# Performance work log

Measured on AMD Instinct MI355X. Metric: run time of the kernel, lower is better.

## Reference

```python
import jax, jax.numpy as jnp
import numpy as np

HID, HEADS = 2048, 16
HD = HID // HEADS  # head_dim = 128
EPS = 1e-6


def rope_tables(head_dim, max_pos, base=10000.0):
    inv = 1.0 / (base ** (jnp.arange(0, head_dim, 2, dtype=jnp.float32) / head_dim))
    t = jnp.arange(max_pos, dtype=jnp.float32)
    freqs = jnp.outer(t, inv)                      # [max_pos, d/2]
    emb = jnp.concatenate([freqs, freqs], axis=-1)  # [max_pos, d]
    return jnp.cos(emb), jnp.sin(emb)


def rotate_half(x):
    x1, x2 = jnp.split(x, 2, axis=-1)
    return jnp.concatenate([-x2, x1], axis=-1)


def lf_gate(x, c1w, c1b, c2w, c2b, rms_w):
    # x: [b, s, h]; prompt phase -> lf1/lf2 caches are zeros -> zero-pad 1 step on time axis
    xt = jnp.transpose(x, (0, 2, 1))[..., None]                 # [b, h, s, 1]
    xt = jnp.pad(xt, ((0, 0), (0, 0), (1, 0), (0, 0)))           # [b, h, s+1, 1]
    dn = ('NCHW', 'OIHW', 'NCHW')
    o1 = jax.lax.conv_general_dilated(xt, c1w, (1, 1), 'VALID', dimension_numbers=dn)
    o1 = o1 + c1b[None, :, None, None]                           # [b, h/2, s, 1]
    o1 = jnp.pad(o1, ((0, 0), (0, 0), (1, 0), (0, 0)))           # [b, h/2, s+1, 1]
    o2 = jax.lax.conv_general_dilated(o1, c2w, (1, 1), 'VALID', dimension_numbers=dn)
    o2 = o2 + c2b[None, :, None, None]                           # [b, h, s, 1]
    y = jnp.transpose(o2[..., 0], (0, 2, 1)) + x                 # residual, [b, s, h]
    var = jnp.mean(y * y, axis=-1, keepdims=True)
    return y * jax.lax.rsqrt(var + EPS) * rms_w


def setup_inputs() -> dict:
    key = jax.random.key(0)
    ks = jax.random.split(key, 10)
    b, s = 2, 2048
    inp = {
        'hidden_states': jax.random.normal(ks[0], (b, s, HID), jnp.float32),
        'positions': jnp.arange(s, dtype=jnp.int32),
        'wq': jax.random.normal(ks[1], (HID, HID), jnp.float32) * 0.02,
        'wk': jax.random.normal(ks[2], (HID, HID), jnp.float32) * 0.02,
        'wv': jax.random.normal(ks[3], (HID, HID), jnp.float32) * 0.02,
        'wo': jax.random.normal(ks[4], (HID, HID), jnp.float32) * 0.02,
        'conv1_w': jax.random.normal(ks[5], (HID // 2, HID, 2, 1), jnp.float32) * 0.02,
        'conv1_b': jnp.zeros((HID // 2,), jnp.float32),
        'conv2_w': jax.random.normal(ks[6], (HID, HID // 2, 2, 1), jnp.float32) * 0.02,
        'conv2_b': jnp.zeros((HID,), jnp.float32),
        'rms_w': jnp.ones((HID,), jnp.float32),
    }
    return inp


def reference(hidden_states, positions, wq, wk, wv, wo, conv1_w, conv1_b, conv2_w, conv2_b, rms_w):
    b, s, _ = hidden_states.shape
    # value projection from raw hidden states (pre-gate)
    v = (hidden_states @ wv).reshape(b, s, HEADS, HD)            # [b, s, H, d]
    # localized-filtering gate (prompt phase: zero caches)
    h = lf_gate(hidden_states, conv1_w, conv1_b, conv2_w, conv2_b, rms_w)
    q = h @ wq                                                   # [b, s, H*d]
    k = h @ wk
    # faithful Yuan quirk: concat q,k then reshape to [b,s,H,2d] and chunk
    qk = jnp.concatenate([q, k], axis=-1).reshape(b, s, HEADS, 2 * HD)
    q, k = jnp.split(qk, 2, axis=-1)                             # each [b, s, H, d]
    # rotary
    cos, sin = rope_tables(HD, 8192)
    c = cos[positions][None, :, None, :]                         # [1, s, 1, d]
    sn = sin[positions][None, :, None, :]
    q = q * c + rotate_half(q) * sn
    k = k * c + rotate_half(k) * sn
    # causal attention (paged attention reduces to this for the prompt)
    scale = HD ** -0.5
    scores = jnp.einsum('bqhd,bkhd->bhqk', q, k) * scale         # [b, H, s, s]
    mask = jnp.tril(jnp.ones((s, s), dtype=bool))
    scores = jnp.where(mask[None, None], scores, jnp.finfo(scores.dtype).min)
    probs = jax.nn.softmax(scores, axis=-1)
    out = jnp.einsum('bhqk,bkhd->bqhd', probs, v).reshape(b, s, HEADS * HD)
    return out @ wo
```

## Files before the change

### kernel.cpp

```cpp
#include <hip/hip_runtime.h>

#define HID 2048
#define HEADS 16
#define HD 128
#define BATCH 2
#define S 2048
#define ROWS (BATCH*S)

typedef short short8 __attribute__((ext_vector_type(8)));
typedef unsigned short ushort4v __attribute__((ext_vector_type(4)));
typedef unsigned short ushort2v __attribute__((ext_vector_type(2)));
typedef float f32x4 __attribute__((ext_vector_type(4)));
typedef __bf16 bf16x8 __attribute__((ext_vector_type(8)));
typedef __bf16 bf16x4 __attribute__((ext_vector_type(4)));

static __device__ __forceinline__ float b2f(unsigned short u) {
  union { float f; unsigned int i; } v; v.i = ((unsigned int)u) << 16; return v.f;
}
static __device__ __forceinline__ unsigned short f2b(float f) {
  union { float f; unsigned int i; } v; v.f = f;
  unsigned int u = v.i;
  unsigned int r = ((u >> 16) & 1u) + 0x7fffu;
  return (unsigned short)((u + r) >> 16);
}

static __device__ __forceinline__ void gload_lds16(const unsigned short* g, unsigned short* l) {
  __builtin_amdgcn_global_load_lds(
      (const __attribute__((address_space(1))) unsigned int*)(const void*)g,
      (__attribute__((address_space(3))) unsigned int*)(void*)l,
      16, 0, 0);
}

__global__ void fill_debug(unsigned short* __restrict__ out, long n) {
  long i = (long)blockIdx.x * blockDim.x + threadIdx.x;
  if (i < n) out[i] = 0x447A;
}

__global__ void prep_combined(const float* __restrict__ c1w, const float* __restrict__ c2w,
                              const float* __restrict__ x, const int* __restrict__ positions,
                              const float* __restrict__ c1b, const float* __restrict__ c2b,
                              const float* __restrict__ rmsw,
                              const float* __restrict__ wq, const float* __restrict__ wk,
                              const float* __restrict__ wv, const float* __restrict__ wo,
                              unsigned short* __restrict__ w1t0, unsigned short* __restrict__ w1t1,
                              unsigned short* __restrict__ w2t0, unsigned short* __restrict__ w2t1,
                              unsigned short* __restrict__ xb,
                              float* __restrict__ ctab, float* __restrict__ stab,
                              unsigned short* __restrict__ c1bb, unsigned short* __restrict__ c2bb,
                              unsigned short* __restrict__ rmswb, unsigned short* __restrict__ zpg,
                              unsigned short* __restrict__ wqkt, unsigned short* __restrict__ wvt,
                              unsigned short* __restrict__ wot) {
  int job = blockIdx.y;
  if (job == 0 || job == 1) {
    const float* w = (job == 0) ? c1w : c2w;
    unsigned short* o0 = (job == 0) ? w1t0 : w2t0;
    unsigned short* o1 = (job == 0) ? w1t1 : w2t1;
    long i = (long)blockIdx.x * 256 + threadIdx.x;
    f32x4 v = *(const f32x4*)(w + i*4);
    ushort2v a = { f2b(v[0]), f2b(v[2]) };
    ushort2v b = { f2b(v[1]), f2b(v[3]) };
    *(ushort2v*)(o0 + i*2) = a;
    *(ushort2v*)(o1 + i*2) = b;
  } else if (job == 2) {
    long i = (long)blockIdx.x * 256 + threadIdx.x;
    #pragma unroll
    for (int rep = 0; rep < 2; ++rep) {
      long idx = i + (long)rep * 1048576L;
      f32x4 v = *(const f32x4*)(x + idx*4);
      ushort4v o = { f2b(v[0]), f2b(v[1]), f2b(v[2]), f2b(v[3]) };
      *(ushort4v*)(xb + idx*4) = o;
    }
  } else if (job == 3) {
    int bx = blockIdx.x;
    if (bx < 512) {
      int t = bx * 4 + (threadIdx.x >> 6);
      int i = threadIdx.x & 63;
      float pos = (float)positions[t];
      float inv = powf(10000.0f, -(float)i / 64.0f);
      float ang = pos * inv;
      float sv, cv;
      sincosf(ang, &sv, &cv);
      ctab[t*64 + i] = cv;
      stab[t*64 + i] = sv;
    } else if (bx < 544) {
      int i = (bx - 512) * 256 + threadIdx.x;
      if (i < 1024) c1bb[i] = f2b(c1b[i]);
      if (i < 2048) { c2bb[i] = f2b(c2b[i]); rmswb[i] = f2b(rmsw[i]); }
      zpg[i] = 0;
    }
  } else {
    __shared__ unsigned short tl[64][73];
    int bx = blockIdx.x;
    int mat = bx >> 10;
    int tx = (bx >> 5) & 31, ty = bx & 31;
    const float* in; unsigned short* out; int perm;
    switch (mat) {
      case 0:  in = wq; out = wqkt;                       perm = 1; break;
      case 1:  in = wk; out = wqkt + (size_t)HID*HID;     perm = 1; break;
      case 2:  in = wv; out = wvt;                        perm = 0; break;
      default: in = wo; out = wot;                        perm = 0; break;
    }
    int n0 = tx * 64, k0 = ty * 64;
    int tid = threadIdx.x;
    int r = tid >> 3, c8 = (tid & 7) * 8;
    #pragma unroll
    for (int j = 0; j < 2; ++j) {
      int rr = r + j*32;
      const float* p = in + (size_t)(k0 + rr)*HID + n0 + c8;
      f32x4 v0 = *(const f32x4*)p;
      f32x4 v1 = *(const f32x4*)(p + 4);
      #pragma unroll
      for (int e = 0; e < 4; ++e) { tl[rr][c8 + e] = f2b(v0[e]); tl[rr][c8 + 4 + e] = f2b(v1[e]); }
    }
    __syncthreads();
    #pragma unroll
    for (int j = 0; j < 2; ++j) {
      int rr = r + j*32;
      int orow = n0 + rr;
      if (perm) {
        int s5 = (orow >> 5) & 3;
        s5 = (s5 == 1) ? 2 : (s5 == 2) ? 1 : s5;
        orow = (orow & ~127) | (s5 << 5) | (orow & 31);
      }
      short8 v;
      #pragma unroll
      for (int e = 0; e < 8; ++e) v[e] = (short)tl[c8 + e][rr];
      *(short8*)(out + (size_t)orow*HID + k0 + c8) = v;
    }
  }
}


static __device__ __forceinline__ int swz_scol(int lane) {
  return (((lane & 7) * 16) ^ (((lane >> 3) & 7) << 4)) >> 1;
}

static __device__ __forceinline__ void rd_af(const unsigned short* Ah, bf16x8 (&afr)[4][2],
                                             int wm, int lr, int col0, int axor) {
  #pragma unroll
  for (int mi = 0; mi < 4; ++mi) {
    const unsigned short* rp = Ah + (wm*64 + mi*16 + lr) * 64;
    #pragma unroll
    for (int kk = 0; kk < 2; ++kk)
      afr[mi][kk] = *(const bf16x8*)(rp + (((kk*64 + col0) ^ axor) >> 1));
  }
}
static __device__ __forceinline__ void rd_bf(const unsigned short* Bh, bf16x8 (&bfr)[2][2],
                                             int wn, int lr, int col0, int axor) {
  #pragma unroll
  for (int ni = 0; ni < 2; ++ni) {
    const unsigned short* rp = Bh + (wn*32 + ni*16 + lr) * 64;
    #pragma unroll
    for (int kk = 0; kk < 2; ++kk)
      bfr[ni][kk] = *(const bf16x8*)(rp + (((kk*64 + col0) ^ axor) >> 1));
  }
}
static __device__ __forceinline__ void mfma16(const bf16x8 (&afr)[4][2], const bf16x8 (&bfr)[2][2],
                                              f32x4 (&ac)[4][2]) {
  #pragma unroll
  for (int kk = 0; kk < 2; ++kk)
    #pragma unroll
    for (int mi = 0; mi < 4; ++mi)
      #pragma unroll
      for (int ni = 0; ni < 2; ++ni)
        ac[mi][ni] = __builtin_amdgcn_mfma_f32_16x16x32_bf16(afr[mi][kk], bfr[ni][kk], ac[mi][ni], 0, 0, 0);
}


struct SPtrs { const unsigned short* p[6]; };

static __device__ __forceinline__ void build_ptrs(SPtrs& sp,
    const unsigned short* Ap, const unsigned short* Bp, int Ksz, int sh,
    int m0, int n0, const unsigned short* zpg, int tid) {
  int lane = tid & 63;
  int scol = swz_scol(lane);
  #pragma unroll
  for (int j = 0; j < 2; ++j) {
    int row = ((tid >> 6) * 2 + j) * 8 + (lane >> 3);
    int gr = m0 + row;
    sp.p[j]     = (sh && ((gr & (S - 1)) == 0)) ? (zpg + scol)
                                                : (Ap + (size_t)(gr - sh)*Ksz + scol);
    sp.p[2 + j] = Bp + (size_t)(n0 + row)*Ksz + scol;
    sp.p[4 + j] = Bp + (size_t)(n0 + 128 + row)*Ksz + scol;
  }
}

static __device__ __forceinline__ void stage6(unsigned short* buf, SPtrs& sp, int tid) {
  int c0 = (tid >> 6) * 1024;
  gload_lds16(sp.p[0], buf + c0);
  gload_lds16(sp.p[1], buf + c0 + 512);
  gload_lds16(sp.p[2], buf + 8192  + c0);
  gload_lds16(sp.p[3], buf + 8192  + c0 + 512);
  gload_lds16(sp.p[4], buf + 16384 + c0);
  gload_lds16(sp.p[5], buf + 16384 + c0 + 512);
  #pragma unroll
  for (int i = 0; i < 6; ++i) sp.p[i] += 64;
}

static __device__ __forceinline__ void gemm8_core(
    unsigned short* lds,
    const unsigned short* __restrict__ A1, const unsigned short* __restrict__ A2,
    const unsigned short* __restrict__ B1, const unsigned short* __restrict__ B2,
    int K1, int K2,
    const unsigned short* __restrict__ bias, const unsigned short* __restrict__ resid,
    void* __restrict__ Cout, int outmode, int N, int m0, int n0,
    int a1shift, const unsigned short* __restrict__ zrow) {
  int tid = threadIdx.x;
  int lane = tid & 63, w = tid >> 6;
  int wm = w >> 2, wn = w & 3;
  int lr = lane & 15, g = lane >> 4;
  int col0 = g * 16;
  int axor = (lr & 7) << 4;
  int nk1 = K1 >> 6;
  int nk = (K1 + K2) >> 6;
  f32x4 acc[2][4][2] = {};
  bf16x8 afr[4][2], bfr0[2][2], bfr1[2][2];

  unsigned short* buf0 = lds;
  unsigned short* buf1 = lds + 24576;
  unsigned short* buf2 = lds + 49152;

  SPtrs sp;
  build_ptrs(sp, A1, B1, K1, a1shift, m0, n0, zrow, tid);

  stage6(buf0, sp, tid);
  stage6(buf1, sp, tid);

  unsigned short* cur = buf0;
  unsigned short* nx1 = buf1;
  unsigned short* nx2 = buf2;
  for (int t = 0; t < nk; ++t) {
    if (t < nk - 1) asm volatile("s_waitcnt vmcnt(6)" ::: "memory");
    else            asm volatile("s_waitcnt vmcnt(0)" ::: "memory");
    __builtin_amdgcn_s_barrier();
    asm volatile("" ::: "memory");

    rd_af(cur,         afr,  wm, lr, col0, axor);
    rd_bf(cur + 8192,  bfr0, wn, lr, col0, axor);
    rd_bf(cur + 16384, bfr1, wn, lr, col0, axor);
    if (t + 2 < nk) {
      if (t + 2 == nk1) build_ptrs(sp, A2, B2, K2, 0, m0, n0, zrow, tid);
      stage6(nx2, sp, tid);
    }
    __builtin_amdgcn_s_setprio(1);
    mfma16(afr, bfr0, acc[0]);
    mfma16(afr, bfr1, acc[1]);
    __builtin_amdgcn_s_setprio(0);

    unsigned short* tmp = cur; cur = nx1; nx1 = nx2; nx2 = tmp;
  }

  #pragma unroll
  for (int qn = 0; qn < 2; ++qn)
    #pragma unroll
    for (int mi = 0; mi < 4; ++mi) {
      int row0 = m0 + wm*64 + mi*16 + g*4;
      #pragma unroll
      for (int ni = 0; ni < 2; ++ni) {
        int col = n0 + qn*128 + wn*32 + ni*16 + lr;
        float bv = bias ? b2f(bias[col]) : 0.f;
        f32x4 a = acc[qn][mi][ni];
        #pragma unroll
        for (int j = 0; j < 4; ++j) {
          size_t idx = (size_t)(row0 + j) * N + col;
          float v = a[j] + bv;
          if (resid) v += b2f(resid[idx]);
          if (outmode == 1) ((float*)Cout)[idx] = v;
          else ((unsigned short*)Cout)[idx] = f2b(v);
        }
      }
    }
}

template<int SHIFT>
__launch_bounds__(512, 1)
__global__ void gemm8_bt(const unsigned short* __restrict__ A1,
                         const unsigned short* __restrict__ A2,
                         const unsigned short* __restrict__ B1,
                         const unsigned short* __restrict__ B2,
                         int K1, int K2,
                         const unsigned short* __restrict__ bias,
                         const unsigned short* __restrict__ resid,
                         void* __restrict__ Cout, int outmode, int N,
                         const unsigned short* __restrict__ zrow) {
  __shared__ __align__(16) unsigned short lds[73728];
  gemm8_core(lds, A1, A2, B1, B2, K1, K2, bias, resid, Cout, outmode, N,
             blockIdx.x*128, blockIdx.y*256, SHIFT, zrow);
}

struct HPtr { const unsigned short* p0; const unsigned short* p1; };
static __device__ __forceinline__ void hinit(HPtr& h, const unsigned short* base,
                                             int row0, int Ksz, int tid) {
  int lane = tid & 63;
  int scol = swz_scol(lane);
  int r0 = ((tid >> 6) * 2) * 8 + (lane >> 3);
  h.p0 = base + (size_t)(row0 + r0) * Ksz + scol;
  h.p1 = base + (size_t)(row0 + r0 + 8) * Ksz + scol;
}
static __device__ __forceinline__ void hinit_sh(HPtr& h, const unsigned short* base,
                                                int row0, int Ksz,
                                                const unsigned short* zpg, int tid) {
  int lane = tid & 63;
  int scol = swz_scol(lane);
  int r0 = ((tid >> 6) * 2) * 8 + (lane >> 3);
  int g0 = row0 + r0, g1 = row0 + r0 + 8;
  h.p0 = ((g0 & (S - 1)) == 0) ? (zpg + scol) : (base + (size_t)(g0 - 1) * Ksz + scol);
  h.p1 = ((g1 & (S - 1)) == 0) ? (zpg + scol) : (base + (size_t)(g1 - 1) * Ksz + scol);
}
static __device__ __forceinline__ void hstage(unsigned short* slot, HPtr& h, int tid) {
  int c0 = (tid >> 6) * 1024;
  gload_lds16(h.p0, slot + c0);
  gload_lds16(h.p1, slot + c0 + 512);
  h.p0 += 64; h.p1 += 64;
}

template<int NKT>
static __device__ __forceinline__ void gemm256_loop(
    unsigned short* lds, HPtr& hA0, HPtr& hA1, HPtr& hB0, HPtr& hB1,
    f32x4 (&acc)[2][2][4][2], int wm, int wn, int lr, int col0, int axor, int tid) {
  bf16x8 af[4][2], bf0[2][2], bf1[2][2];
  const int nk = NKT;
  hstage(lds + 0,             hA0, tid);
  hstage(lds + 8192,          hA1, tid);
  hstage(lds + 16384,         hB0, tid);
  hstage(lds + 24576,         hB1, tid);
  hstage(lds + 32768 + 0,     hA0, tid);
  hstage(lds + 32768 + 16384, hB0, tid);
  hstage(lds + 32768 + 24576, hB1, tid);
  asm volatile("s_waitcnt vmcnt(6)" ::: "memory");
  __builtin_amdgcn_s_barrier();
  asm volatile("" ::: "memory");

  for (int t = 0; t < nk; ++t) {
    unsigned short* cur = lds + (t & 1) * 32768;
    unsigned short* oth = lds + ((t & 1) ^ 1) * 32768;

    rd_af(cur,         af,  wm, lr, col0, axor);
    rd_bf(cur + 16384, bf0, wn, lr, col0, axor);
    if (t + 1 < nk) hstage(oth + 8192, hA1, tid);
    __builtin_amdgcn_s_barrier();
    asm volatile("s_waitcnt lgkmcnt(0)" ::: "memory");
    __builtin_amdgcn_s_setprio(1);
    mfma16(af, bf0, acc[0][0]);
    __builtin_amdgcn_s_setprio(0);
    __builtin_amdgcn_s_barrier();

    rd_bf(cur + 24576, bf1, wn, lr, col0, axor);
    if (t + 2 < nk) hstage(cur, hA0, tid);
    __builtin_amdgcn_s_barrier();
    asm volatile("s_waitcnt lgkmcnt(0)" ::: "memory");
    __builtin_amdgcn_s_setprio(1);
    mfma16(af, bf1, acc[0][1]);
    __builtin_amdgcn_s_setprio(0);
    __builtin_amdgcn_s_barrier();

    rd_af(cur + 8192, af, wm, lr, col0, axor);
    if (t + 2 < nk) hstage(cur + 16384, hB0, tid);
    __builtin_amdgcn_s_barrier();
    asm volatile("s_waitcnt lgkmcnt(0)" ::: "memory");
    __builtin_amdgcn_s_setprio(1);
    mfma16(af, bf1, acc[1][1]);
    __builtin_amdgcn_s_setprio(0);
    __builtin_amdgcn_s_barrier();

    if (t + 2 < nk) hstage(cur + 24576, hB1, tid);
    __builtin_amdgcn_s_barrier();
    asm volatile("s_waitcnt lgkmcnt(0)" ::: "memory");
    __builtin_amdgcn_s_setprio(1);
    mfma16(af, bf0, acc[1][0]);
    __builtin_amdgcn_s_setprio(0);
    if (t + 2 < nk) asm volatile("s_waitcnt vmcnt(6)" ::: "memory");
    else            asm volatile("s_waitcnt vmcnt(0)" ::: "memory");
    __builtin_amdgcn_s_barrier();
    asm volatile("" ::: "memory");
  }
}

__launch_bounds__(512, 1)
__global__ void gemm256_qk_rope(const unsigned short* __restrict__ A,
                                const unsigned short* __restrict__ B,
                                const float* __restrict__ ctab,
                                const float* __restrict__ stab,
                                unsigned short* __restrict__ qr,
                                unsigned short* __restrict__ kr) {
  __shared__ __align__(16) unsigned short lds[65536];
  int tid = threadIdx.x;
  int lane = tid & 63, w = tid >> 6;
  int wm = w >> 2, wn = w & 3;
  int lr = lane & 15, g = lane >> 4;
  int col0 = g * 16;
  int axor = (lr & 7) << 4;
  int nwg = gridDim.x * gridDim.y;
  int lin = blockIdx.y * gridDim.x + blockIdx.x;
  int cpx = nwg >> 3;
  int swz = (lin & 7) * cpx + (lin >> 3);
  int m0 = (swz % gridDim.x) * 256, n0 = (swz / gridDim.x) * 256;
  f32x4 acc[2][2][4][2] = {};

  HPtr hA0, hA1, hB0, hB1;
  hinit(hA0, A, m0,       2048, tid);
  hinit(hA1, A, m0 + 128, 2048, tid);
  hinit(hB0, B, n0,       2048, tid);
  hinit(hB1, B, n0 + 128, 2048, tid);
  gemm256_loop<32>(lds, hA0, hA1, hB0, hB1, acc, wm, wn, lr, col0, axor, tid);

  float* L = (float*)lds;
  const float SC = 0.08838834764831845f * 1.44269504088896340f;
  int h = n0 >> 8;
  int r2 = tid >> 2;
  int ib = (tid & 3) * 16;
  #pragma unroll
  for (int qm = 0; qm < 2; ++qm) {
    #pragma unroll
    for (int qn = 0; qn < 2; ++qn) {
      #pragma unroll
      for (int mi = 0; mi < 4; ++mi)
        #pragma unroll
        for (int ni = 0; ni < 2; ++ni) {
          f32x4 a = acc[qm][qn][mi][ni];
          #pragma unroll
          for (int j = 0; j < 4; ++j)
            L[(wm*64 + mi*16 + g*4 + j)*132 + wn*32 + ni*16 + lr] = a[j];
        }
      __syncthreads();
      int rowg = m0 + qm*128 + r2;
      int t = rowg & (S - 1);
      size_t o = (size_t)rowg * HID + (size_t)h * HD;
      unsigned short* dst = (qn == 0) ? qr : kr;
      float sc = (qn == 0) ? SC : 1.0f;
      #pragma unroll
      for (int v4 = 0; v4 < 4; ++v4) {
        ushort4v w1, w2;
        #pragma unroll
        for (int e = 0; e < 4; ++e) {
          int i = ib + v4*4 + e;
          int pc = (i & 31) + ((i >> 5) << 6);
          float x1 = L[r2*132 + pc];
          float x2 = L[r2*132 + pc + 32];
          float cc = ctab[t*64 + i];
          float sn = stab[t*64 + i];
          w1[e] = f2b((x1*cc - x2*sn) * sc);
          w2[e] = f2b((x2*cc + x1*sn) * sc);
        }
        *(ushort4v*)(dst + o + ib + v4*4)      = w1;
        *(ushort4v*)(dst + o + 64 + ib + v4*4) = w2;
      }
      __syncthreads();
    }
  }
}

__launch_bounds__(512, 1)
__global__ void gemm256_trio(const unsigned short* __restrict__ xb,
                             const unsigned short* __restrict__ w1t0,
                             const unsigned short* __restrict__ w1t1,
                             const unsigned short* __restrict__ wvt,
                             unsigned short* __restrict__ o1a,
                             unsigned short* __restrict__ o1b,
                             unsigned short* __restrict__ vtg,
                             const unsigned short* __restrict__ zpg) {
  __shared__ __align__(16) unsigned short lds[68608];
  int tid = threadIdx.x;
  int lane = tid & 63, w = tid >> 6;
  int wm = w >> 2, wn = w & 3;
  int lr = lane & 15, g = lane >> 4;
  int col0 = g * 16;
  int axor = (lr & 7) << 4;
  int lin = blockIdx.x;
  int swz = (lin & 7) * 32 + (lin >> 3);
  int job, s;
  if (swz < 64)       { job = 0; s = swz; }
  else if (swz < 128) { job = 1; s = swz - 64; }
  else                { job = 2; s = swz - 128; }
  int m0 = (s & 15) * 256;
  int n0 = (s >> 4) * 256;
  f32x4 acc[2][2][4][2] = {};

  HPtr hA0, hA1, hB0, hB1;
  if (job == 0) { hinit_sh(hA0, xb, m0, 2048, zpg, tid); hinit_sh(hA1, xb, m0 + 128, 2048, zpg, tid); }
  else          { hinit(hA0, xb, m0, 2048, tid);         hinit(hA1, xb, m0 + 128, 2048, tid); }
  const unsigned short* B = (job == 0) ? w1t0 : (job == 1) ? w1t1 : wvt;
  hinit(hB0, B, n0,       2048, tid);
  hinit(hB1, B, n0 + 128, 2048, tid);
  gemm256_loop<32>(lds, hA0, hA1, hB0, hB1, acc, wm, wn, lr, col0, axor, tid);

  if (job < 2) {
    unsigned short* C = (job == 0) ? o1a : o1b;
    #pragma unroll
    for (int qm = 0; qm < 2; ++qm)
      #pragma unroll
      for (int mi = 0; mi < 4; ++mi) {
        int row0 = m0 + qm*128 + wm*64 + mi*16 + g*4;
        #pragma unroll
        for (int qn = 0; qn < 2; ++qn)
          #pragma unroll
          for (int ni = 0; ni < 2; ++ni) {
            int col = n0 + qn*128 + wn*32 + ni*16 + lr;
            f32x4 a = acc[qm][qn][mi][ni];
            #pragma unroll
            for (int j = 0; j < 4; ++j)
              C[(size_t)(row0 + j) * 1024 + col] = f2b(a[j]);
          }
      }
  } else {
    float* L = (float*)lds;
    #pragma unroll
    for (int qm = 0; qm < 2; ++qm) {
      #pragma unroll
      for (int qn = 0; qn < 2; ++qn) {
        #pragma unroll
        for (int mi = 0; mi < 4; ++mi)
          #pragma unroll
          for (int ni = 0; ni < 2; ++ni) {
            f32x4 a = acc[qm][qn][mi][ni];
            #pragma unroll
            for (int j = 0; j < 4; ++j)
              L[(wm*64 + mi*16 + g*4 + j)*133 + wn*32 + ni*16 + lr] = a[j];
          }
        __syncthreads();
        int rowg0 = m0 + qm*128;
        int bb = rowg0 >> 11;
        int s0q = rowg0 & (S - 1);
        int dg0 = n0 + qn*128;
        #pragma unroll
        for (int cl = 0; cl < 16; ++cl) {
          int col = w*16 + cl;
          size_t vbase = ((size_t)bb * HID + dg0 + col) * S + s0q;
          vtg[vbase + lane]      = f2b(L[lane*133 + col]);
          vtg[vbase + 64 + lane] = f2b(L[(64 + lane)*133 + col]);
        }
        __syncthreads();
      }
    }
  }
}

__launch_bounds__(512, 1)
__global__ void gemm256_duo(const unsigned short* __restrict__ o1,
                            const unsigned short* __restrict__ w2t0,
                            const unsigned short* __restrict__ w2t1,
                            unsigned short* __restrict__ pA,
                            unsigned short* __restrict__ pB,
                            const unsigned short* __restrict__ zpg) {
  __shared__ __align__(16) unsigned short lds[65536];
  int tid = threadIdx.x;
  int lane = tid & 63, w = tid >> 6;
  int wm = w >> 2, wn = w & 3;
  int lr = lane & 15, g = lane >> 4;
  int col0 = g * 16;
  int axor = (lr & 7) << 4;
  int lin = blockIdx.x;
  int swz = (lin & 7) * 32 + (lin >> 3);
  int job = swz >> 7;
  int s = swz & 127;
  int m0 = (s & 15) * 256;
  int n0 = (s >> 4) * 256;
  f32x4 acc[2][2][4][2] = {};

  HPtr hA0, hA1, hB0, hB1;
  if (job == 0) { hinit_sh(hA0, o1, m0, 1024, zpg, tid); hinit_sh(hA1, o1, m0 + 128, 1024, zpg, tid); }
  else          { hinit(hA0, o1, m0, 1024, tid);         hinit(hA1, o1, m0 + 128, 1024, tid); }
  const unsigned short* B = (job == 0) ? w2t0 : w2t1;
  hinit(hB0, B, n0,       1024, tid);
  hinit(hB1, B, n0 + 128, 1024, tid);
  gemm256_loop<16>(lds, hA0, hA1, hB0, hB1, acc, wm, wn, lr, col0, axor, tid);

  unsigned short* C = (job == 0) ? pA : pB;
  #pragma unroll
  for (int qm = 0; qm < 2; ++qm)
    #pragma unroll
    for (int mi = 0; mi < 4; ++mi) {
      int row0 = m0 + qm*128 + wm*64 + mi*16 + g*4;
      #pragma unroll
      for (int qn = 0; qn < 2; ++qn)
        #pragma unroll
        for (int ni = 0; ni < 2; ++ni) {
          int col = n0 + qn*128 + wn*32 + ni*16 + lr;
          f32x4 a = acc[qm][qn][mi][ni];
          #pragma unroll
          for (int j = 0; j < 4; ++j)
            C[(size_t)(row0 + j) * HID + col] = f2b(a[j]);
        }
    }
}

__global__ void add_bias(const unsigned short* __restrict__ a,
                         const unsigned short* __restrict__ b,
                         const unsigned short* __restrict__ bias,
                         unsigned short* __restrict__ o) {
  long i8 = ((long)blockIdx.x * 256 + threadIdx.x) * 8;
  short8 va = *(const short8*)(a + i8);
  short8 vb = *(const short8*)(b + i8);
  short8 wb = *(const short8*)(bias + (i8 & 1023));
  short8 vo;
  #pragma unroll
  for (int e = 0; e < 8; ++e)
    vo[e] = (short)f2b(b2f((unsigned short)va[e]) + b2f((unsigned short)vb[e])
                       + b2f((unsigned short)wb[e]));
  *(short8*)(o + i8) = vo;
}

__global__ void rms_fuse(const unsigned short* __restrict__ pA,
                         const unsigned short* __restrict__ pB,
                         const unsigned short* __restrict__ bias,
                         const unsigned short* __restrict__ resid,
                         const unsigned short* __restrict__ w,
                         unsigned short* __restrict__ out) {
  int r = blockIdx.x;
  int c8 = threadIdx.x * 8;
  size_t base = (size_t)r * HID + c8;
  short8 va = *(const short8*)(pA + base);
  short8 vb = *(const short8*)(pB + base);
  short8 vx = *(const short8*)(resid + base);
  short8 vbi = *(const short8*)(bias + c8);
  float f[8];
  float ss = 0.f;
  #pragma unroll
  for (int e = 0; e < 8; ++e) {
    f[e] = b2f((unsigned short)va[e]) + b2f((unsigned short)vb[e])
         + b2f((unsigned short)vbi[e]) + b2f((unsigned short)vx[e]);
    ss += f[e]*f[e];
  }
  #pragma unroll
  for (int o = 32; o; o >>= 1) ss += __shfl_xor(ss, o);
  __shared__ float red[4];
  if ((threadIdx.x & 63) == 0) red[threadIdx.x >> 6] = ss;
  __syncthreads();
  float tot = red[0] + red[1] + red[2] + red[3];
  float scale = rsqrtf(tot / (float)HID + 1e-6f);
  short8 wv = *(const short8*)(w + c8);
  short8 o8;
  #pragma unroll
  for (int e = 0; e < 8; ++e) o8[e] = (short)f2b(f[e] * scale * b2f((unsigned short)wv[e]));
  *(short8*)(out + base) = o8;
}

#define KT 64

static __device__ __forceinline__ void attn_pass(
    int qt, int b, int h, unsigned short* lds,
    const unsigned short* __restrict__ Qr, const unsigned short* __restrict__ Kr,
    const unsigned short* __restrict__ Vt, unsigned short* __restrict__ Out) {
  int tid = threadIdx.x, lane = tid & 63, w = tid >> 6;
  int q0 = qt * 64;
  size_t bS = (size_t)b * S;
  size_t ho = (size_t)h * HD;
  int lr = lane & 15, g = lane >> 4;
  int rsw = (lane & 7) << 3;
  __syncthreads();
  bf16x8 bq[4];
  {
    int qrow = q0 + w*16 + lr;
    const unsigned short* qp = Qr + (bS + qrow)*HID + ho + g*8;
    #pragma unroll
    for (int kk = 0; kk < 4; ++kk) bq[kk] = *(const bf16x8*)(qp + kk*32);
  }
  const unsigned short* kp[4];
  const unsigned short* vp[4];
  #pragma unroll
  for (int j = 0; j < 4; ++j) {
    int c = w*4 + j;
    int rk = c*4 + (lane >> 4);
    int sck = ((lane & 15) * 8) ^ ((rk & 7) << 3);
    kp[j] = Kr + (bS + rk)*HID + ho + sck;
    int rv = c*8 + (lane >> 3);
    int scv = ((lane & 7) * 8) ^ ((rv & 7) << 3);
    vp[j] = Vt + ((size_t)b*HID + ho + rv)*S + scv;
  }
  int cdst = (w*4) * 512;
  unsigned short* curK = lds;
  unsigned short* curV = lds + 8192;
  unsigned short* nxtK = lds + 16384;
  unsigned short* nxtV = lds + 24576;
  #pragma unroll
  for (int j = 0; j < 4; ++j) {
    gload_lds16(kp[j], curK + cdst + j*512);
    gload_lds16(vp[j], curV + cdst + j*512);
    kp[j] += (size_t)KT * HID;
    vp[j] += KT;
  }
  f32x4 o[8] = {};
  float m = -1e30f, l = 0.f;
  unsigned short* PlW = lds + 32768 + w*1024;
  int ntiles = qt + 1;
  for (int kt = 0; kt < ntiles; ++kt) {
    asm volatile("s_waitcnt vmcnt(0)" ::: "memory");
    __builtin_amdgcn_s_barrier();
    asm volatile("" ::: "memory");
    if (kt + 1 < ntiles) {
      #pragma unroll
      for (int j = 0; j < 4; ++j) {
        gload_lds16(kp[j], nxtK + cdst + j*512);
        gload_lds16(vp[j], nxtV + cdst + j*512);
        kp[j] += (size_t)KT * HID;
        vp[j] += KT;
      }
    }
    f32x4 st[4] = {};
    __builtin_amdgcn_s_setprio(1);
    #pragma unroll
    for (int kk = 0; kk < 4; ++kk) {
      #pragma unroll
      for (int mi = 0; mi < 4; ++mi) {
        bf16x8 a = *(const bf16x8*)(&curK[(mi*16 + lr)*128 + ((kk*32 + g*8) ^ rsw)]);
        st[mi] = __builtin_amdgcn_mfma_f32_16x16x32_bf16(a, bq[kk], st[mi], 0, 0, 0);
      }
    }
    __builtin_amdgcn_s_setprio(0);
    bool lastt = (kt == ntiles - 1);
    float tm = -1e30f;
    #pragma unroll
    for (int mi = 0; mi < 4; ++mi)
      #pragma unroll
      for (int r = 0; r < 4; ++r) {
        float v = st[mi][r];
        if (lastt && (mi*16 + 4*g + r) > (w*16 + lr)) v = -1e30f;
        st[mi][r] = v;
        tm = fmaxf(tm, v);
      }
    tm = fmaxf(tm, __shfl_xor(tm, 16));
    tm = fmaxf(tm, __shfl_xor(tm, 32));
    if (!__all(tm - m <= 11.5f)) {
      float mn = fmaxf(m, tm);
      float sc = exp2f(m - mn);
      float s0 = __shfl(sc, 4*g+0), s1 = __shfl(sc, 4*g+1);
      float s2 = __shfl(sc, 4*g+2), s3 = __shfl(sc, 4*g+3);
      #pragma unroll
      for (int ni = 0; ni < 8; ++ni) {
        o[ni][0] *= s0; o[ni][1] *= s1; o[ni][2] *= s2; o[ni][3] *= s3;
      }
      l *= sc;
      m = mn;
    }
    float ts = 0.f;
    __bf16 pbf[4][4];
    #pragma unroll
    for (int mi = 0; mi < 4; ++mi)
      #pragma unroll
      for (int r = 0; r < 4; ++r) {
        float p = exp2f(st[mi][r] - m);
        ts += p;
        pbf[mi][r] = (__bf16)p;
      }
    ts += __shfl_xor(ts, 16);
    ts += __shfl_xor(ts, 32);
    l += ts;
    #pragma unroll
    for (int mi = 0; mi < 4; ++mi) {
      bf16x4 pk = { pbf[mi][0], pbf[mi][1], pbf[mi][2], pbf[mi][3] };
      *(bf16x4*)(&PlW[lr*64 + ((mi*16 + 4*g) ^ rsw)]) = pk;
    }
    asm volatile("" ::: "memory");
    __builtin_amdgcn_s_setprio(1);
    #pragma unroll
    for (int kk = 0; kk < 2; ++kk) {
      int pc = (kk*32 + g*8) ^ rsw;
      bf16x8 a = *(const bf16x8*)(&PlW[lr*64 + pc]);
      #pragma unroll
      for (int ni = 0; ni < 8; ++ni) {
        bf16x8 bv = *(const bf16x8*)(&curV[(ni*16 + lr)*64 + pc]);
        o[ni] = __builtin_amdgcn_mfma_f32_16x16x32_bf16(a, bv, o[ni], 0, 0, 0);
      }
    }
    __builtin_amdgcn_s_setprio(0);
    unsigned short* t0 = curK; curK = nxtK; nxtK = t0;
    unsigned short* t1 = curV; curV = nxtV; nxtV = t1;
  }
  float l0 = __shfl(l, 4*g+0), l1 = __shfl(l, 4*g+1);
  float l2 = __shfl(l, 4*g+2), l3 = __shfl(l, 4*g+3);
  float i0 = 1.f/l0, i1 = 1.f/l1, i2 = 1.f/l2, i3 = 1.f/l3;
  int rbase = q0 + w*16 + 4*g;
  #pragma unroll
  for (int ni = 0; ni < 8; ++ni) {
    size_t cbase = ho + ni*16 + lr;
    Out[(bS + rbase + 0)*HID + cbase] = f2b(o[ni][0]*i0);
    Out[(bS + rbase + 1)*HID + cbase] = f2b(o[ni][1]*i1);
    Out[(bS + rbase + 2)*HID + cbase] = f2b(o[ni][2]*i2);
    Out[(bS + rbase + 3)*HID + cbase] = f2b(o[ni][3]*i3);
  }
}

__launch_bounds__(256, 2)
__global__ void attn_mfma(const unsigned short* __restrict__ Qr,
                          const unsigned short* __restrict__ Kr,
                          const unsigned short* __restrict__ Vt,
                          unsigned short* __restrict__ Out) {
  __shared__ __align__(16) unsigned short lds[36864];
  int bh = blockIdx.x;
  int b = bh >> 4, h = bh & 15;
  int by = blockIdx.y;
  attn_pass(31 - by, b, h, lds, Qr, Kr, Vt, Out);
  attn_pass(by,      b, h, lds, Qr, Kr, Vt, Out);
}

extern "C" void kernel_launch(void* const* d_in, const int* in_sizes, int n_in,
                              void* d_out, int out_size, void* d_ws, size_t ws_size,
                              hipStream_t stream) {
  const float* x_raw   = (const float*)d_in[0];
  const int* positions = (const int*)d_in[1];
  const float* wq_raw  = (const float*)d_in[2];
  const float* wk_raw  = (const float*)d_in[3];
  const float* wv_raw  = (const float*)d_in[4];
  const float* wo_raw  = (const float*)d_in[5];
  const float* c1w_raw = (const float*)d_in[6];
  const float* c1b_raw = (const float*)d_in[7];
  const float* c2w_raw = (const float*)d_in[8];
  const float* c2b_raw = (const float*)d_in[9];
  const float* rms_raw = (const float*)d_in[10];

  const size_t WS_NEEDED = 140000000;
  if (ws_size < WS_NEEDED) {
    long n = (long)out_size;
    fill_debug<<<dim3((unsigned)((n + 255) / 256)), dim3(256), 0, stream>>>((unsigned short*)d_out, n);
    return;
  }

  char* ws = (char*)d_ws;
  size_t off = 0;
  auto alloc = [&](size_t bytes) { char* p = ws + off; off += (bytes + 255) & ~(size_t)255; return p; };
  float* ctab          = (float*)alloc((size_t)S*64*4);
  float* stab          = (float*)alloc((size_t)S*64*4);
  unsigned short* wqkt = (unsigned short*)alloc((size_t)2*HID*HID*2);
  unsigned short* wvt  = (unsigned short*)alloc((size_t)HID*HID*2);
  unsigned short* wot  = (unsigned short*)alloc((size_t)HID*HID*2);
  unsigned short* w1t0 = (unsigned short*)alloc((size_t)1024*HID*2);
  unsigned short* w1t1 = (unsigned short*)alloc((size_t)1024*HID*2);
  unsigned short* w2t0 = (unsigned short*)alloc((size_t)HID*1024*2);
  unsigned short* w2t1 = (unsigned short*)alloc((size_t)HID*1024*2);
  unsigned short* xb   = (unsigned short*)alloc((size_t)ROWS*HID*2);
  unsigned short* qrb  = (unsigned short*)alloc((size_t)ROWS*HID*2);
  unsigned short* o1   = (unsigned short*)alloc((size_t)ROWS*1024*2);
  unsigned short* yb   = (unsigned short*)alloc((size_t)ROWS*HID*2);
  unsigned short* hg   = (unsigned short*)alloc((size_t)ROWS*HID*2);
  unsigned short* qkf  = (unsigned short*)alloc((size_t)ROWS*2*HID*2);
  unsigned short* vtg  = (unsigned short*)alloc((size_t)BATCH*HID*S*2);
  unsigned short* c1bb = (unsigned short*)alloc(1024*2);
  unsigned short* c2bb = (unsigned short*)alloc(2048*2);
  unsigned short* rmswb= (unsigned short*)alloc(2048*2);
  unsigned short* zpg  = (unsigned short*)alloc(8192*2);
  unsigned short* krr  = xb;
  unsigned short* attn = yb;
  unsigned short* o1a  = qkf;
  unsigned short* o1b  = qkf + (size_t)ROWS*1024;
  unsigned short* cpA  = qkf;
  unsigned short* cpB  = qkf + (size_t)ROWS*HID;

  dim3 b256(256);
  dim3 b512(512);
  prep_combined<<<dim3(4096, 5), b256, 0, stream>>>(
      c1w_raw, c2w_raw, x_raw, positions, c1b_raw, c2b_raw, rms_raw,
      wq_raw, wk_raw, wv_raw, wo_raw,
      w1t0, w1t1, w2t0, w2t1, xb, ctab, stab, c1bb, c2bb, rmswb, zpg,
      wqkt, wvt, wot);
  gemm256_trio<<<dim3(256), b512, 0, stream>>>(xb, w1t0, w1t1, wvt, o1a, o1b, vtg, zpg);
  add_bias<<<dim3(ROWS*1024/8/256), b256, 0, stream>>>(o1a, o1b, c1bb, o1);
  gemm256_duo<<<dim3(256), b512, 0, stream>>>(o1, w2t0, w2t1, cpA, cpB, zpg);
  rms_fuse<<<dim3(ROWS), b256, 0, stream>>>(cpA, cpB, c2bb, xb, rmswb, hg);
  gemm256_qk_rope<<<dim3(ROWS/256, (2*HID)/256), b512, 0, stream>>>(hg, wqkt, ctab, stab, qrb, krr);
  attn_mfma<<<dim3(BATCH*HEADS, 16), b256, 0, stream>>>(qrb, krr, vtg, attn);
  gemm8_bt<0><<<dim3(ROWS/128, HID/256), b512, 0, stream>>>(attn, attn, wot, wot, HID, 0, nullptr, nullptr, d_out, 1, HID, nullptr);
}
```

Baseline: 329.9 us.

## Switch attention to 32x32x16 MFMA with 128-row query tiles and register P

Rewrites the attention pass to use 32x32x16 bf16 MFMA instead of 16x16x32. Each wave now owns 32 query rows, so a block covers 128 query rows, and the grid's y dimension is halved. The probability tile is passed to the PV matmul through lane shuffles instead of a round trip through LDS, which removes the P buffer from shared memory. Each K/V tile loaded is reused across twice as many queries, but each wave holds more accumulator registers, the grid has fewer blocks, and more work is wasted on masked diagonal tiles.

```diff
diff --git a/kernel.cpp b/kernel.cpp
--- a/kernel.cpp
+++ b/kernel.cpp
@@ -11,8 +11,10 @@
 typedef unsigned short ushort4v __attribute__((ext_vector_type(4)));
 typedef unsigned short ushort2v __attribute__((ext_vector_type(2)));
 typedef float f32x4 __attribute__((ext_vector_type(4)));
+typedef float f32x16 __attribute__((ext_vector_type(16)));
 typedef __bf16 bf16x8 __attribute__((ext_vector_type(8)));
 typedef __bf16 bf16x4 __attribute__((ext_vector_type(4)));
+typedef __bf16 bf16x2 __attribute__((ext_vector_type(2)));
 
 static __device__ __forceinline__ float b2f(unsigned short u) {
   union { float f; unsigned int i; } v; v.i = ((unsigned int)u) << 16; return v.f;
@@ -637,23 +639,22 @@
 
 #define KT 64
 
-static __device__ __forceinline__ void attn_pass(
+static __device__ __forceinline__ void attn32_pass(
     int qt, int b, int h, unsigned short* lds,
     const unsigned short* __restrict__ Qr, const unsigned short* __restrict__ Kr,
     const unsigned short* __restrict__ Vt, unsigned short* __restrict__ Out) {
   int tid = threadIdx.x, lane = tid & 63, w = tid >> 6;
-  int q0 = qt * 64;
+  int q0w = qt * 128 + w * 32;
   size_t bS = (size_t)b * S;
   size_t ho = (size_t)h * HD;
-  int lr = lane & 15, g = lane >> 4;
+  int l31 = lane & 31, hi = lane >> 5;
   int rsw = (lane & 7) << 3;
   __syncthreads();
-  bf16x8 bq[4];
+  bf16x8 bq[8];
   {
-    int qrow = q0 + w*16 + lr;
-    const unsigned short* qp = Qr + (bS + qrow)*HID + ho + g*8;
-    #pragma unroll
-    for (int kk = 0; kk < 4; ++kk) bq[kk] = *(const bf16x8*)(qp + kk*32);
+    const unsigned short* qp = Qr + (bS + q0w + l31)*HID + ho + hi*8;
+    #pragma unroll
+    for (int kk = 0; kk < 8; ++kk) bq[kk] = *(const bf16x8*)(qp + kk*16);
   }
   const unsigned short* kp[4];
   const unsigned short* vp[4];
@@ -679,10 +680,9 @@
     kp[j] += (size_t)KT * HID;
     vp[j] += KT;
   }
-  f32x4 o[8] = {};
+  f32x16 o2[4] = {};
   float m = -1e30f, l = 0.f;
-  unsigned short* PlW = lds + 32768 + w*1024;
-  int ntiles = qt + 1;
+  int ntiles = 2*qt + 2;
   for (int kt = 0; kt < ntiles; ++kt) {
     asm volatile("s_waitcnt vmcnt(0)" ::: "memory");
     __builtin_amdgcn_s_barrier();
@@ -696,87 +696,99 @@
         vp[j] += KT;
       }
     }
-    f32x4 st[4] = {};
+    f32x16 st0 = {}, st1 = {};
     __builtin_amdgcn_s_setprio(1);
     #pragma unroll
-    for (int kk = 0; kk < 4; ++kk) {
-      #pragma unroll
-      for (int mi = 0; mi < 4; ++mi) {
-        bf16x8 a = *(const bf16x8*)(&curK[(mi*16 + lr)*128 + ((kk*32 + g*8) ^ rsw)]);
-        st[mi] = __builtin_amdgcn_mfma_f32_16x16x32_bf16(a, bq[kk], st[mi], 0, 0, 0);
-      }
+    for (int kk = 0; kk < 8; ++kk) {
+      bf16x8 a0 = *(const bf16x8*)(&curK[(l31)*128      + ((kk*16 + hi*8) ^ rsw)]);
+      bf16x8 a1 = *(const bf16x8*)(&curK[(32 + l31)*128 + ((kk*16 + hi*8) ^ rsw)]);
+      st0 = __builtin_amdgcn_mfma_f32_32x32x16_bf16(a0, bq[kk], st0, 0, 0, 0);
+      st1 = __builtin_amdgcn_mfma_f32_32x32x16_bf16(a1, bq[kk], st1, 0, 0, 0);
     }
     __builtin_amdgcn_s_setprio(0);
-    bool lastt = (kt == ntiles - 1);
+    int kbase = kt * 64;
     float tm = -1e30f;
-    #pragma unroll
-    for (int mi = 0; mi < 4; ++mi)
-      #pragma unroll
-      for (int r = 0; r < 4; ++r) {
-        float v = st[mi][r];
-        if (lastt && (mi*16 + 4*g + r) > (w*16 + lr)) v = -1e30f;
-        st[mi][r] = v;
-        tm = fmaxf(tm, v);
-      }
-    tm = fmaxf(tm, __shfl_xor(tm, 16));
+    if (kbase + 63 > q0w) {
+      int qg = q0w + l31;
+      #pragma unroll
+      for (int r = 0; r < 16; ++r) {
+        int crow = (r&3) + 8*(r>>2) + 4*hi;
+        if (kbase + crow > qg)      st0[r] = -1e30f;
+        if (kbase + 32 + crow > qg) st1[r] = -1e30f;
+        tm = fmaxf(tm, fmaxf(st0[r], st1[r]));
+      }
+    } else {
+      #pragma unroll
+      for (int r = 0; r < 16; ++r) tm = fmaxf(tm, fmaxf(st0[r], st1[r]));
+    }
     tm = fmaxf(tm, __shfl_xor(tm, 32));
     if (!__all(tm - m <= 11.5f)) {
       float mn = fmaxf(m, tm);
       float sc = exp2f(m - mn);
-      float s0 = __shfl(sc, 4*g+0), s1 = __shfl(sc, 4*g+1);
-      float s2 = __shfl(sc, 4*g+2), s3 = __shfl(sc, 4*g+3);
-      #pragma unroll
-      for (int ni = 0; ni < 8; ++ni) {
-        o[ni][0] *= s0; o[ni][1] *= s1; o[ni][2] *= s2; o[ni][3] *= s3;
+      #pragma unroll
+      for (int r = 0; r < 16; ++r) {
+        int crow = (r&3) + 8*(r>>2) + 4*hi;
+        float scv = __shfl(sc, crow);
+        #pragma unroll
+        for (int ni = 0; ni < 4; ++ni) o2[ni][r] *= scv;
       }
       l *= sc;
       m = mn;
     }
     float ts = 0.f;
-    __bf16 pbf[4][4];
-    #pragma unroll
-    for (int mi = 0; mi < 4; ++mi)
-      #pragma unroll
-      for (int r = 0; r < 4; ++r) {
-        float p = exp2f(st[mi][r] - m);
-        ts += p;
-        pbf[mi][r] = (__bf16)p;
-      }
-    ts += __shfl_xor(ts, 16);
+    unsigned int u0[8], u1[8];
+    #pragma unroll
+    for (int j = 0; j < 8; ++j) {
+      float a0 = exp2f(st0[2*j] - m), b0 = exp2f(st0[2*j+1] - m);
+      float a1 = exp2f(st1[2*j] - m), b1 = exp2f(st1[2*j+1] - m);
+      ts += a0 + b0 + a1 + b1;
+      union { bf16x2 v; unsigned int ui; } p0, p1;
+      p0.v = bf16x2{(__bf16)a0, (__bf16)b0};
+      p1.v = bf16x2{(__bf16)a1, (__bf16)b1};
+      u0[j] = p0.ui; u1[j] = p1.ui;
+    }
     ts += __shfl_xor(ts, 32);
     l += ts;
-    #pragma unroll
-    for (int mi = 0; mi < 4; ++mi) {
-      bf16x4 pk = { pbf[mi][0], pbf[mi][1], pbf[mi][2], pbf[mi][3] };
-      *(bf16x4*)(&PlW[lr*64 + ((mi*16 + 4*g) ^ rsw)]) = pk;
-    }
-    asm volatile("" ::: "memory");
+    unsigned int x0[8], x1[8];
+    #pragma unroll
+    for (int j = 0; j < 8; ++j) {
+      x0[j] = (unsigned int)__shfl_xor((int)u0[j], 32);
+      x1[j] = (unsigned int)__shfl_xor((int)u1[j], 32);
+    }
     __builtin_amdgcn_s_setprio(1);
     #pragma unroll
-    for (int kk = 0; kk < 2; ++kk) {
-      int pc = (kk*32 + g*8) ^ rsw;
-      bf16x8 a = *(const bf16x8*)(&PlW[lr*64 + pc]);
-      #pragma unroll
-      for (int ni = 0; ni < 8; ++ni) {
-        bf16x8 bv = *(const bf16x8*)(&curV[(ni*16 + lr)*64 + pc]);
-        o[ni] = __builtin_amdgcn_mfma_f32_16x16x32_bf16(a, bv, o[ni], 0, 0, 0);
+    for (int s = 0; s < 4; ++s) {
+      int j16 = s & 1;
+      unsigned int w0, w1, w2, w3;
+      if (s < 2) {
+        if (hi == 0) { w0=u0[4*j16];   w1=u0[4*j16+1]; w2=x0[4*j16];   w3=x0[4*j16+1]; }
+        else         { w0=x0[4*j16+2]; w1=x0[4*j16+3]; w2=u0[4*j16+2]; w3=u0[4*j16+3]; }
+      } else {
+        if (hi == 0) { w0=u1[4*j16];   w1=u1[4*j16+1]; w2=x1[4*j16];   w3=x1[4*j16+1]; }
+        else         { w0=x1[4*j16+2]; w1=x1[4*j16+3]; w2=u1[4*j16+2]; w3=u1[4*j16+3]; }
+      }
+      union { unsigned int ui[4]; bf16x8 v; } pa;
+      pa.ui[0]=w0; pa.ui[1]=w1; pa.ui[2]=w2; pa.ui[3]=w3;
+      #pragma unroll
+      for (int ni = 0; ni < 4; ++ni) {
+        int d = ni*32 + l31;
+        bf16x8 bv = *(const bf16x8*)(&curV[d*64 + ((s*16 + hi*8) ^ rsw)]);
+        o2[ni] = __builtin_amdgcn_mfma_f32_32x32x16_bf16(pa.v, bv, o2[ni], 0, 0, 0);
       }
     }
     __builtin_amdgcn_s_setprio(0);
     unsigned short* t0 = curK; curK = nxtK; nxtK = t0;
     unsigned short* t1 = curV; curV = nxtV; nxtV = t1;
   }
-  float l0 = __shfl(l, 4*g+0), l1 = __shfl(l, 4*g+1);
-  float l2 = __shfl(l, 4*g+2), l3 = __shfl(l, 4*g+3);
-  float i0 = 1.f/l0, i1 = 1.f/l1, i2 = 1.f/l2, i3 = 1.f/l3;
-  int rbase = q0 + w*16 + 4*g;
-  #pragma unroll
-  for (int ni = 0; ni < 8; ++ni) {
-    size_t cbase = ho + ni*16 + lr;
-    Out[(bS + rbase + 0)*HID + cbase] = f2b(o[ni][0]*i0);
-    Out[(bS + rbase + 1)*HID + cbase] = f2b(o[ni][1]*i1);
-    Out[(bS + rbase + 2)*HID + cbase] = f2b(o[ni][2]*i2);
-    Out[(bS + rbase + 3)*HID + cbase] = f2b(o[ni][3]*i3);
+  float invl = 1.f / l;
+  #pragma unroll
+  for (int r = 0; r < 16; ++r) {
+    int crow = (r&3) + 8*(r>>2) + 4*hi;
+    float iv = __shfl(invl, crow);
+    size_t rowbase = (bS + q0w + crow)*HID + ho + l31;
+    #pragma unroll
+    for (int ni = 0; ni < 4; ++ni)
+      Out[rowbase + ni*32] = f2b(o2[ni][r] * iv);
   }
 }
 
@@ -785,12 +797,12 @@
                           const unsigned short* __restrict__ Kr,
                           const unsigned short* __restrict__ Vt,
                           unsigned short* __restrict__ Out) {
-  __shared__ __align__(16) unsigned short lds[36864];
+  __shared__ __align__(16) unsigned short lds[32768];
   int bh = blockIdx.x;
   int b = bh >> 4, h = bh & 15;
   int by = blockIdx.y;
-  attn_pass(31 - by, b, h, lds, Qr, Kr, Vt, Out);
-  attn_pass(by,      b, h, lds, Qr, Kr, Vt, Out);
+  attn32_pass(15 - by, b, h, lds, Qr, Kr, Vt, Out);
+  attn32_pass(by,      b, h, lds, Qr, Kr, Vt, Out);
 }
 
 extern "C" void kernel_launch(void* const* d_in, const int* in_sizes, int n_in,
@@ -857,6 +869,6 @@
   gemm256_duo<<<dim3(256), b512, 0, stream>>>(o1, w2t0, w2t1, cpA, cpB, zpg);
   rms_fuse<<<dim3(ROWS), b256, 0, stream>>>(cpA, cpB, c2bb, xb, rmswb, hg);
   gemm256_qk_rope<<<dim3(ROWS/256, (2*HID)/256), b512, 0, stream>>>(hg, wqkt, ctab, stab, qrb, krr);
-  attn_mfma<<<dim3(BATCH*HEADS, 16), b256, 0, stream>>>(qrb, krr, vtg, attn);
+  attn_mfma<<<dim3(BATCH*HEADS, 8), b256, 0, stream>>>(qrb, krr, vtg, attn);
   gemm8_bt<0><<<dim3(ROWS/128, HID/256), b512, 0, stream>>>(attn, attn, wot, wot, HID, 0, nullptr, nullptr, d_out, 1, HID, nullptr);
 }
```

Result: slower. 336.7 us (+2.1%).
